# Performance work log

Hardware: AMD Instinct MI355X
Metric: run time of the kernel (lower is better)

## Reference

```python
import jax, jax.numpy as jnp
import numpy as np

B, T, C, H = 8, 2048, 1024, 64

def setup_inputs() -> dict:
    key = jax.random.key(0)
    kx, kk, kq, kv = jax.random.split(key, 4)
    x = jax.random.normal(kx, (B, T, C), dtype=jnp.float32)
    # nn.Linear(n_embed, head_size, bias=False) weights stored as [C, H] (already transposed)
    s = 1.0 / np.sqrt(C)
    Wk = jax.random.normal(kk, (C, H), dtype=jnp.float32) * s
    Wq = jax.random.normal(kq, (C, H), dtype=jnp.float32) * s
    Wv = jax.random.normal(kv, (C, H), dtype=jnp.float32) * s
    return {"x": x, "Wk": Wk, "Wq": Wq, "Wv": Wv}

def reference(x, Wk, Wq, Wv):
    Bq, Tq, Cq = x.shape
    k = jnp.einsum('btc,ch->bth', x, Wk)
    q = jnp.einsum('btc,ch->bth', x, Wq)
    v = jnp.einsum('btc,ch->bth', x, Wv)
    # NOTE: faithful to source, which MULTIPLIES by C**0.5 (not 1/sqrt(head_size))
    wei = jnp.einsum('bth,bsh->bts', q, k) * (Cq ** 0.5)  # [B,T,T]
    causal = jnp.tril(jnp.ones((Tq, Tq), dtype=bool))
    wei = jnp.where(causal, wei, -jnp.inf)
    wei = jax.nn.softmax(wei, axis=-1)
    out = jnp.einsum('bts,bsh->bth', wei, v)  # [B,T,H]
    return out
```

## Files before the change

### kernel.cpp

```cpp
#include <hip/hip_runtime.h>
#include <hip/hip_bf16.h>

#define TSEQ 2048
#define CDIM 1024
#define HDIM 64
#define NROW (8 * 2048)

typedef __attribute__((ext_vector_type(8))) short bf16x8;
typedef __attribute__((ext_vector_type(4))) float f32x4;
typedef __attribute__((ext_vector_type(4))) unsigned int u32x4;

__device__ __forceinline__ unsigned short f2bf(float f) {
    return __builtin_bit_cast(unsigned short, __float2bfloat16(f));
}
__device__ __forceinline__ float bf2f(unsigned short h) {
    unsigned int u = ((unsigned int)h) << 16;
    return __builtin_bit_cast(float, u);
}
__device__ __forceinline__ void split2(float v, unsigned short& h, unsigned short& l) {
    __hip_bfloat16 bh = __float2bfloat16(v);
    h = __builtin_bit_cast(unsigned short, bh);
    l = f2bf(v - __bfloat162float(bh));
}
__device__ __forceinline__ f32x4 mfma16(bf16x8 a, bf16x8 b, f32x4 c) {
    return __builtin_amdgcn_mfma_f32_16x16x32_bf16(a, b, c, 0, 0, 0);
}
__device__ __forceinline__ void gload_lds16(const unsigned short* g, unsigned short* l) {
    __builtin_amdgcn_global_load_lds(
        (const __attribute__((address_space(1))) unsigned int*)(g),
        (__attribute__((address_space(3))) unsigned int*)(l), 16, 0, 0);
}
__device__ __forceinline__ void gload_lds16f(const float* g, float* l) {
    __builtin_amdgcn_global_load_lds(
        (const __attribute__((address_space(1))) unsigned int*)(g),
        (__attribute__((address_space(3))) unsigned int*)(l), 16, 0, 0);
}

__global__ __launch_bounds__(256) void w_prep(
    const float* __restrict__ Wk, const float* __restrict__ Wq, const float* __restrict__ Wv,
    unsigned short* __restrict__ wThi, unsigned short* __restrict__ wTlo)
{
    __shared__ float tile[64][65];
    const int mm = blockIdx.x >> 4, kt = blockIdx.x & 15;
    const float* __restrict__ W = (mm == 0) ? Wk : (mm == 1) ? Wq : Wv;
    const int t = threadIdx.x;
    #pragma unroll
    for (int s = 0; s < 4; s++) {
        const int f = t + 256 * s;
        const int r = f >> 4, cq = f & 15;
        const float4 wv = *reinterpret_cast<const float4*>(&W[(long)(kt * 64 + r) * HDIM + 4 * cq]);
        tile[4 * cq + 0][r] = wv.x; tile[4 * cq + 1][r] = wv.y;
        tile[4 * cq + 2][r] = wv.z; tile[4 * cq + 3][r] = wv.w;
    }
    __syncthreads();
    const int n = t >> 2, seg = t & 3;
    unsigned short hi[16], lo[16];
    #pragma unroll
    for (int u = 0; u < 16; u++) split2(tile[n][16 * seg + u], hi[u], lo[u]);
    const long base = (long)(mm * 64 + n) * CDIM + kt * 64 + 16 * seg;
    *reinterpret_cast<uint4*>(&wThi[base + 0]) = *reinterpret_cast<uint4*>(&hi[0]);
    *reinterpret_cast<uint4*>(&wThi[base + 8]) = *reinterpret_cast<uint4*>(&hi[8]);
    *reinterpret_cast<uint4*>(&wTlo[base + 0]) = *reinterpret_cast<uint4*>(&lo[0]);
    *reinterpret_cast<uint4*>(&wTlo[base + 8]) = *reinterpret_cast<uint4*>(&lo[8]);
}

__global__ __launch_bounds__(256, 4) void proj_mfma(
    const float* __restrict__ x,
    const unsigned short* __restrict__ wThi, const unsigned short* __restrict__ wTlo,
    unsigned short* __restrict__ khi, unsigned short* __restrict__ klo,
    unsigned short* __restrict__ qhi, unsigned short* __restrict__ qlo,
    unsigned short* __restrict__ vt)
{
    extern __shared__ __align__(16) unsigned char smem[];
    const int t = threadIdx.x;
    const int lane = t & 63, w = t >> 6;
    const int r15 = lane & 15, g = lane >> 4;
    const int wr = w >> 1, wc = w & 1;
    const int bb8 = blockIdx.x & 7;
    const int u = blockIdx.x >> 3;
    const int jj = u >> 1, nh = u & 1;
    const long rowbase = (long)bb8 * TSEQ + jj * 64;

    long wsrc[3];
    #pragma unroll
    for (int q = 0; q < 3; q++) {
        const int s = t + 256 * q;
        const int row = s >> 3, gr = s & 7;
        wsrc[q] = (long)(nh * 96 + row) * CDIM + ((gr ^ (row & 7)) << 3);
    }
    long xsrc[4];
    #pragma unroll
    for (int q = 0; q < 4; q++) {
        const int s = t + 256 * q;
        const int row = s >> 4, gr = s & 15;
        xsrc[q] = (rowbase + row) * CDIM + ((gr ^ (row & 15)) << 2);
    }

    f32x4 acc[2][3];
    #pragma unroll
    for (int mt = 0; mt < 2; mt++)
        #pragma unroll
        for (int nt = 0; nt < 3; nt++) acc[mt][nt] = (f32x4){0.f, 0.f, 0.f, 0.f};

    auto stage = [&](int buf, int kc) {
        unsigned char* b = smem + buf * 40960;
        #pragma unroll
        for (int q = 0; q < 3; q++) {
            gload_lds16(wThi + wsrc[q] + kc, (unsigned short*)(b + (t + 256 * q) * 16));
            gload_lds16(wTlo + wsrc[q] + kc, (unsigned short*)(b + 12288 + (t + 256 * q) * 16));
        }
        #pragma unroll
        for (int q = 0; q < 4; q++)
            gload_lds16f(x + xsrc[q] + kc, (float*)(b + 24576 + (t + 256 * q) * 16));
    };

    auto compute = [&](int buf) {
        const unsigned short* wb = (const unsigned short*)(smem + buf * 40960);
        const float* xb = (const float*)(smem + buf * 40960 + 24576);
        bf16x8 ah[2][2], al[2][2];
        #pragma unroll
        for (int mt = 0; mt < 2; mt++) {
            const int rx = 32 * wr + 16 * mt + r15;
            #pragma unroll
            for (int ks = 0; ks < 2; ks++) {
                const f32x4 a0 = *reinterpret_cast<const f32x4*>(
                    xb + rx * 64 + (((8 * ks + 2 * g + 0) ^ r15) << 2));
                const f32x4 a1 = *reinterpret_cast<const f32x4*>(
                    xb + rx * 64 + (((8 * ks + 2 * g + 1) ^ r15) << 2));
                unsigned short h0,h1,h2,h3,h4,h5,h6,h7, l0,l1,l2,l3,l4,l5,l6,l7;
                split2(a0.x, h0, l0); split2(a0.y, h1, l1); split2(a0.z, h2, l2); split2(a0.w, h3, l3);
                split2(a1.x, h4, l4); split2(a1.y, h5, l5); split2(a1.z, h6, l6); split2(a1.w, h7, l7);
                ah[mt][ks] = (bf16x8){(short)h0,(short)h1,(short)h2,(short)h3,(short)h4,(short)h5,(short)h6,(short)h7};
                al[mt][ks] = (bf16x8){(short)l0,(short)l1,(short)l2,(short)l3,(short)l4,(short)l5,(short)l6,(short)l7};
            }
        }
        #pragma unroll
        for (int nt = 0; nt < 3; nt++) {
            const int rw = (3 * wc + nt) * 16 + r15;
            #pragma unroll
            for (int ks = 0; ks < 2; ks++) {
                const int go = (((4 * ks + g) ^ (rw & 7)) << 3);
                const bf16x8 bh = *reinterpret_cast<const bf16x8*>(wb + rw * 64 + go);
                const bf16x8 bl = *reinterpret_cast<const bf16x8*>(wb + 6144 + rw * 64 + go);
                #pragma unroll
                for (int mt = 0; mt < 2; mt++) {
                    acc[mt][nt] = mfma16(ah[mt][ks], bh, acc[mt][nt]);
                    acc[mt][nt] = mfma16(al[mt][ks], bh, acc[mt][nt]);
                    acc[mt][nt] = mfma16(ah[mt][ks], bl, acc[mt][nt]);
                }
            }
        }
    };

    stage(0, 0);
    __syncthreads();
    for (int j = 0; j < 16; ++j) {
        const int buf = j & 1;
        if (j < 15) stage(buf ^ 1, (j + 1) * 64);
        compute(buf);
        __syncthreads();
    }

    #pragma unroll
    for (int nt = 0; nt < 3; nt++) {
        const int ntg = 6 * nh + 3 * wc + nt;
        const int mat = ntg >> 2;
        const int colin = (ntg & 3) * 16 + r15;
        #pragma unroll
        for (int mt = 0; mt < 2; mt++) {
            const int rl = 32 * wr + 16 * mt + 4 * g;
            if (mat == 0) {
                #pragma unroll
                for (int reg = 0; reg < 4; reg++) {
                    unsigned short h, l;
                    split2(acc[mt][nt][reg], h, l);
                    const long idx = (rowbase + rl + reg) * HDIM + colin;
                    khi[idx] = h; klo[idx] = l;
                }
            } else if (mat == 1) {
                #pragma unroll
                for (int reg = 0; reg < 4; reg++) {
                    unsigned short h, l;
                    split2(acc[mt][nt][reg] * 32.0f, h, l);
                    const long idx = (rowbase + rl + reg) * HDIM + colin;
                    qhi[idx] = h; qlo[idx] = l;
                }
            } else {
                ushort4 pk;
                pk.x = f2bf(acc[mt][nt][0]); pk.y = f2bf(acc[mt][nt][1]);
                pk.z = f2bf(acc[mt][nt][2]); pk.w = f2bf(acc[mt][nt][3]);
                const long idx = ((long)bb8 * 64 + colin) * TSEQ + jj * 64 + rl;
                *reinterpret_cast<ushort4*>(&vt[idx]) = pk;
            }
        }
    }
}

__global__ __launch_bounds__(256, 3) void attn_part(
    const unsigned short* __restrict__ khi, const unsigned short* __restrict__ klo,
    const unsigned short* __restrict__ qhi, const unsigned short* __restrict__ qlo,
    const unsigned short* __restrict__ vt,
    float* __restrict__ po, float* __restrict__ pm, float* __restrict__ pl, int nsplit)
{
    __shared__ __align__(16) unsigned short ldsbuf[2][3 * 4096];
    const int t = threadIdx.x, w = t >> 6, lane = t & 63;
    const int r15 = lane & 15, g = lane >> 4;
    const int id = blockIdx.x;
    const int b = id & 7;
    const int u = id >> 3;
    const int t5 = u & 31, p = u >> 5;
    int j = (t5 & 1) ? 31 - (t5 >> 1) : (t5 >> 1);
    if (p & 1) j = 31 - j;
    const int n = j + 1;
    const int s = (p * n) / nsplit, e = ((p + 1) * n) / nsplit;
    const int pidx = (b * 32 + j) * nsplit + p;

    if (s >= e) {
        const int rr = t >> 2, cq = (t & 3) * 16;
        if ((t & 3) == 0) { pm[pidx * 64 + rr] = -3e38f; pl[pidx * 64 + rr] = 0.f; }
        const f32x4 z = (f32x4){0.f, 0.f, 0.f, 0.f};
        float* dst = &po[((long)pidx * 64 + rr) * 64 + cq];
        #pragma unroll
        for (int q = 0; q < 4; q++) *reinterpret_cast<f32x4*>(dst + 4 * q) = z;
        return;
    }

    const int row0 = t >> 3;
    const int ce = (((t & 7) ^ (row0 & 7)) << 3);
    const long bkey = (long)b * TSEQ;
    const long vrow = ((long)b * 64 + row0) * TSEQ;
    unsigned short* const lbT = &ldsbuf[0][0];

    auto stage = [&](int cur, int kb) {
        unsigned short* lb = lbT + cur * (3 * 4096) + t * 8;
        const long kgo  = (bkey + (long)kb * 64 + row0) * HDIM + ce;
        const long kgo2 = kgo + 32 * HDIM;
        const long vgo  = vrow + (long)kb * 64 + ce;
        const long vgo2 = vgo + 32L * TSEQ;
        gload_lds16(khi + kgo,  lb);
        gload_lds16(khi + kgo2, lb + 2048);
        gload_lds16(klo + kgo,  lb + 4096);
        gload_lds16(klo + kgo2, lb + 6144);
        gload_lds16(vt  + vgo,  lb + 8192);
        gload_lds16(vt  + vgo2, lb + 10240);
    };

    const long qrow = bkey + (long)j * 64 + 16 * w + r15;
    bf16x8 Qh[2], Ql[2];
    #pragma unroll
    for (int ks = 0; ks < 2; ks++) {
        Qh[ks] = *reinterpret_cast<const bf16x8*>(&qhi[qrow * HDIM + 32 * ks + 8 * g]);
        Ql[ks] = *reinterpret_cast<const bf16x8*>(&qlo[qrow * HDIM + 32 * ks + 8 * g]);
    }

    f32x4 o[4];
    #pragma unroll
    for (int ht = 0; ht < 4; ht++) o[ht] = (f32x4){0.f, 0.f, 0.f, 0.f};
    float m = -3e38f, lsum = 0.f;
    const int sw = (r15 & 7) << 4;
    const int c0 = ((16 * g) ^ sw) >> 1;
    const int c1 = ((16 * g + 64) ^ sw) >> 1;
    const int la = 16 * ((2 * g) & 3) + r15;
    const int lb_ = 16 * ((2 * g + 1) & 3) + r15;
    const int msel = g >> 1;

    stage(0, s);
    __syncthreads();

    for (int kb = s; kb < e; ++kb) {
        const int cur = (kb - s) & 1;
        if (kb + 1 < e) stage(cur ^ 1, kb + 1);
        const unsigned short* Kh = lbT + cur * (3 * 4096);
        const unsigned short* Kl = Kh + 4096;
        const unsigned short* Vb = Kh + 8192;
        const bool diag = (kb == j);

        f32x4 sc[4];
        #pragma unroll
        for (int mt = 0; mt < 4; mt++) {
            const bool valid = !diag || (mt <= w);
            f32x4 sv = valid ? (f32x4){0.f, 0.f, 0.f, 0.f}
                             : (f32x4){-1e30f, -1e30f, -1e30f, -1e30f};
            if (valid) {
                const int rb = (16 * mt + r15) * 64;
                const bf16x8 ah0 = *reinterpret_cast<const bf16x8*>(&Kh[rb + c0]);
                const bf16x8 ah1 = *reinterpret_cast<const bf16x8*>(&Kh[rb + c1]);
                const bf16x8 al0 = *reinterpret_cast<const bf16x8*>(&Kl[rb + c0]);
                const bf16x8 al1 = *reinterpret_cast<const bf16x8*>(&Kl[rb + c1]);
                sv = mfma16(ah0, Qh[0], sv);
                sv = mfma16(ah0, Ql[0], sv);
                sv = mfma16(al0, Qh[0], sv);
                sv = mfma16(ah1, Qh[1], sv);
                sv = mfma16(ah1, Ql[1], sv);
                sv = mfma16(al1, Qh[1], sv);
                if (diag && mt == w) {
                    #pragma unroll
                    for (int reg = 0; reg < 4; reg++)
                        if (4 * g + reg > r15) sv[reg] = -1e30f;
                }
            }
            sc[mt] = sv;
        }

        float bml = -3e38f;
        #pragma unroll
        for (int mt = 0; mt < 4; mt++)
            bml = fmaxf(bml, fmaxf(fmaxf(sc[mt][0], sc[mt][1]), fmaxf(sc[mt][2], sc[mt][3])));
        if (!__all(bml - m <= 8.0f)) {
            float bm = fmaxf(bml, __shfl_xor(bml, 16));
            bm = fmaxf(bm, __shfl_xor(bm, 32));
            const float mnew = fmaxf(m, bm);
            const float corr = __expf(m - mnew);
            lsum *= corr;
            #pragma unroll
            for (int ht = 0; ht < 4; ht++) o[ht] *= corr;
            m = mnew;
        }
        unsigned int pk[4][2];
        #pragma unroll
        for (int mt = 0; mt < 4; mt++) {
            const float p0 = __expf(sc[mt][0] - m);
            const float p1 = __expf(sc[mt][1] - m);
            const float p2 = __expf(sc[mt][2] - m);
            const float p3 = __expf(sc[mt][3] - m);
            lsum += (p0 + p1) + (p2 + p3);
            pk[mt][0] = (unsigned int)f2bf(p0) | ((unsigned int)f2bf(p1) << 16);
            pk[mt][1] = (unsigned int)f2bf(p2) | ((unsigned int)f2bf(p3) << 16);
        }
        #pragma unroll
        for (int ks = 0; ks < 2; ks++) {
            const int w0a = __shfl((int)pk[2 * ks + 0][0], la);
            const int w0b = __shfl((int)pk[2 * ks + 1][0], la);
            const int w1a = __shfl((int)pk[2 * ks + 0][1], la);
            const int w1b = __shfl((int)pk[2 * ks + 1][1], la);
            const int w2a = __shfl((int)pk[2 * ks + 0][0], lb_);
            const int w2b = __shfl((int)pk[2 * ks + 1][0], lb_);
            const int w3a = __shfl((int)pk[2 * ks + 0][1], lb_);
            const int w3b = __shfl((int)pk[2 * ks + 1][1], lb_);
            const u32x4 wv = {
                (unsigned int)(msel ? w0b : w0a), (unsigned int)(msel ? w1b : w1a),
                (unsigned int)(msel ? w2b : w2a), (unsigned int)(msel ? w3b : w3a)};
            const bf16x8 pb = __builtin_bit_cast(bf16x8, wv);
            const int cc = ks ? c1 : c0;
            #pragma unroll
            for (int ht = 0; ht < 4; ht++) {
                const bf16x8 av = *reinterpret_cast<const bf16x8*>(&Vb[(16 * ht + r15) * 64 + cc]);
                o[ht] = mfma16(av, pb, o[ht]);
            }
        }
        __syncthreads();
    }

    lsum += __shfl_xor(lsum, 16);
    lsum += __shfl_xor(lsum, 32);
    if (g == 0) { pm[pidx * 64 + 16 * w + r15] = m; pl[pidx * 64 + 16 * w + r15] = lsum; }
    #pragma unroll
    for (int ht = 0; ht < 4; ht++)
        *reinterpret_cast<f32x4*>(&po[((long)pidx * 64 + 16 * w + r15) * 64 + 16 * ht + 4 * g]) = o[ht];
}

__global__ __launch_bounds__(256) void attn_comb(
    const float* __restrict__ po, const float* __restrict__ pm, const float* __restrict__ pl,
    float* __restrict__ out, int nsplit)
{
    const int t = threadIdx.x;
    const int b = blockIdx.x & 7, j = blockIdx.x >> 3;
    const int r = t >> 2, cq = (t & 3) * 16;
    const int base = (b * 32 + j) * nsplit;

    float M = -3e38f;
    for (int p = 0; p < nsplit; ++p) M = fmaxf(M, pm[(base + p) * 64 + r]);
    float L = 0.f;
    f32x4 acc[4];
    #pragma unroll
    for (int q = 0; q < 4; q++) acc[q] = (f32x4){0.f, 0.f, 0.f, 0.f};
    for (int p = 0; p < nsplit; ++p) {
        const float wp = __expf(pm[(base + p) * 64 + r] - M);
        L += wp * pl[(base + p) * 64 + r];
        const float* src = &po[((long)(base + p) * 64 + r) * 64 + cq];
        #pragma unroll
        for (int q = 0; q < 4; q++) acc[q] += wp * *reinterpret_cast<const f32x4*>(src + 4 * q);
    }
    const float inv = 1.0f / L;
    float* dst = &out[((long)b * TSEQ + j * 64 + r) * HDIM + cq];
    #pragma unroll
    for (int q = 0; q < 4; q++) *reinterpret_cast<f32x4*>(dst + 4 * q) = acc[q] * inv;
}

extern "C" void kernel_launch(void* const* d_in, const int* in_sizes, int n_in,
                              void* d_out, int out_size, void* d_ws, size_t ws_size,
                              hipStream_t stream) {
    const float* x  = (const float*)d_in[0];
    const float* Wk = (const float*)d_in[1];
    const float* Wq = (const float*)d_in[2];
    const float* Wv = (const float*)d_in[3];
    float* outp = (float*)d_out;

    const size_t SZ = (size_t)NROW * HDIM;
    unsigned short* ws   = (unsigned short*)d_ws;
    unsigned short* khi  = ws;
    unsigned short* klo  = ws + 1 * SZ;
    unsigned short* qhi  = ws + 2 * SZ;
    unsigned short* qlo  = ws + 3 * SZ;
    unsigned short* vt   = ws + 4 * SZ;
    unsigned short* wThi = ws + 5 * SZ;
    unsigned short* wTlo = ws + 5 * SZ + 192 * 1024;

    const size_t base_bytes = (5 * SZ + 2 * 192 * 1024) * sizeof(unsigned short);
    int nsplit = 4;
    while (nsplit > 1 && base_bytes + (size_t)nsplit * 4325376 > ws_size) nsplit >>= 1;

    float* po = (float*)((char*)d_ws + base_bytes);
    float* pm = po + (size_t)256 * 64 * 64 * nsplit;
    float* pl = pm + (size_t)256 * 64 * nsplit;

    w_prep<<<48, 256, 0, stream>>>(Wk, Wq, Wv, wThi, wTlo);
    proj_mfma<<<512, 256, 81920, stream>>>(x, wThi, wTlo, khi, klo, qhi, qlo, vt);
    attn_part<<<dim3(256 * nsplit), 256, 0, stream>>>(khi, klo, qhi, qlo, vt, po, pm, pl, nsplit);
    attn_comb<<<256, 256, 0, stream>>>(po, pm, pl, outp, nsplit);
}
```

Before: 65.10 us.

## Triple-buffer projection GEMM with 32-wide K slices and vmcnt-based waits

The projection kernel now moves through K in 32-wide slices held in a 3-slot LDS ring, replacing the 64-wide double buffer. It waits on explicit vmcnt counts plus raw barriers, so two slices stay in flight while the current one is computed. The swizzles are reworked for the narrower rows, and shared memory per block drops from 80 KB to 60 KB, which may allow more resident blocks. The cost is twice as many loop iterations and barriers, and the hand-set vmcnt values must match the number of loads issued per stage exactly.

```diff
diff --git a/kernel.cpp b/kernel.cpp
--- a/kernel.cpp
+++ b/kernel.cpp
@@ -81,19 +81,22 @@
     const int jj = u >> 1, nh = u & 1;
     const long rowbase = (long)bb8 * TSEQ + jj * 64;
 
-    long wsrc[3];
+    const unsigned short* wsp[3];
     #pragma unroll
     for (int q = 0; q < 3; q++) {
         const int s = t + 256 * q;
+        const int lo = (s >= 384);
+        const int s3 = s - 384 * lo;
+        const int row = s3 >> 2, gr = s3 & 3;
+        wsp[q] = (lo ? wTlo : wThi) + (long)(nh * 96 + row) * CDIM
+               + ((gr ^ ((row >> 1) & 3)) << 3);
+    }
+    long xsrc[2];
+    #pragma unroll
+    for (int q = 0; q < 2; q++) {
+        const int s = t + 256 * q;
         const int row = s >> 3, gr = s & 7;
-        wsrc[q] = (long)(nh * 96 + row) * CDIM + ((gr ^ (row & 7)) << 3);
-    }
-    long xsrc[4];
-    #pragma unroll
-    for (int q = 0; q < 4; q++) {
-        const int s = t + 256 * q;
-        const int row = s >> 4, gr = s & 15;
-        xsrc[q] = (rowbase + row) * CDIM + ((gr ^ (row & 15)) << 2);
+        xsrc[q] = (rowbase + row) * CDIM + ((gr ^ (row & 7)) << 2);
     }
 
     f32x4 acc[2][3];
@@ -102,63 +105,63 @@
         #pragma unroll
         for (int nt = 0; nt < 3; nt++) acc[mt][nt] = (f32x4){0.f, 0.f, 0.f, 0.f};
 
-    auto stage = [&](int buf, int kc) {
-        unsigned char* b = smem + buf * 40960;
-        #pragma unroll
-        for (int q = 0; q < 3; q++) {
-            gload_lds16(wThi + wsrc[q] + kc, (unsigned short*)(b + (t + 256 * q) * 16));
-            gload_lds16(wTlo + wsrc[q] + kc, (unsigned short*)(b + 12288 + (t + 256 * q) * 16));
-        }
-        #pragma unroll
-        for (int q = 0; q < 4; q++)
-            gload_lds16f(x + xsrc[q] + kc, (float*)(b + 24576 + (t + 256 * q) * 16));
+    auto stage = [&](int sl, int kc) {
+        unsigned char* b = smem + sl * 20480;
+        #pragma unroll
+        for (int q = 0; q < 3; q++)
+            gload_lds16(wsp[q] + kc, (unsigned short*)(b + (t + 256 * q) * 16));
+        #pragma unroll
+        for (int q = 0; q < 2; q++)
+            gload_lds16f(x + xsrc[q] + kc, (float*)(b + 12288 + (t + 256 * q) * 16));
     };
 
-    auto compute = [&](int buf) {
-        const unsigned short* wb = (const unsigned short*)(smem + buf * 40960);
-        const float* xb = (const float*)(smem + buf * 40960 + 24576);
-        bf16x8 ah[2][2], al[2][2];
+    auto compute = [&](int sl) {
+        const unsigned short* wb = (const unsigned short*)(smem + sl * 20480);
+        const float* xb = (const float*)(smem + sl * 20480 + 12288);
+        bf16x8 ah[2], al[2];
         #pragma unroll
         for (int mt = 0; mt < 2; mt++) {
             const int rx = 32 * wr + 16 * mt + r15;
-            #pragma unroll
-            for (int ks = 0; ks < 2; ks++) {
-                const f32x4 a0 = *reinterpret_cast<const f32x4*>(
-                    xb + rx * 64 + (((8 * ks + 2 * g + 0) ^ r15) << 2));
-                const f32x4 a1 = *reinterpret_cast<const f32x4*>(
-                    xb + rx * 64 + (((8 * ks + 2 * g + 1) ^ r15) << 2));
-                unsigned short h0,h1,h2,h3,h4,h5,h6,h7, l0,l1,l2,l3,l4,l5,l6,l7;
-                split2(a0.x, h0, l0); split2(a0.y, h1, l1); split2(a0.z, h2, l2); split2(a0.w, h3, l3);
-                split2(a1.x, h4, l4); split2(a1.y, h5, l5); split2(a1.z, h6, l6); split2(a1.w, h7, l7);
-                ah[mt][ks] = (bf16x8){(short)h0,(short)h1,(short)h2,(short)h3,(short)h4,(short)h5,(short)h6,(short)h7};
-                al[mt][ks] = (bf16x8){(short)l0,(short)l1,(short)l2,(short)l3,(short)l4,(short)l5,(short)l6,(short)l7};
-            }
+            const int r7 = rx & 7;
+            const f32x4 a0 = *reinterpret_cast<const f32x4*>(
+                xb + rx * 32 + (((2 * g + 0) ^ r7) << 2));
+            const f32x4 a1 = *reinterpret_cast<const f32x4*>(
+                xb + rx * 32 + (((2 * g + 1) ^ r7) << 2));
+            unsigned short h0,h1,h2,h3,h4,h5,h6,h7, l0,l1,l2,l3,l4,l5,l6,l7;
+            split2(a0.x, h0, l0); split2(a0.y, h1, l1); split2(a0.z, h2, l2); split2(a0.w, h3, l3);
+            split2(a1.x, h4, l4); split2(a1.y, h5, l5); split2(a1.z, h6, l6); split2(a1.w, h7, l7);
+            ah[mt] = (bf16x8){(short)h0,(short)h1,(short)h2,(short)h3,(short)h4,(short)h5,(short)h6,(short)h7};
+            al[mt] = (bf16x8){(short)l0,(short)l1,(short)l2,(short)l3,(short)l4,(short)l5,(short)l6,(short)l7};
         }
         #pragma unroll
         for (int nt = 0; nt < 3; nt++) {
             const int rw = (3 * wc + nt) * 16 + r15;
+            const int go = ((g ^ ((rw >> 1) & 3)) << 3);
+            const bf16x8 bh = *reinterpret_cast<const bf16x8*>(wb + rw * 32 + go);
+            const bf16x8 bl = *reinterpret_cast<const bf16x8*>(wb + 3072 + rw * 32 + go);
             #pragma unroll
-            for (int ks = 0; ks < 2; ks++) {
-                const int go = (((4 * ks + g) ^ (rw & 7)) << 3);
-                const bf16x8 bh = *reinterpret_cast<const bf16x8*>(wb + rw * 64 + go);
-                const bf16x8 bl = *reinterpret_cast<const bf16x8*>(wb + 6144 + rw * 64 + go);
-                #pragma unroll
-                for (int mt = 0; mt < 2; mt++) {
-                    acc[mt][nt] = mfma16(ah[mt][ks], bh, acc[mt][nt]);
-                    acc[mt][nt] = mfma16(al[mt][ks], bh, acc[mt][nt]);
-                    acc[mt][nt] = mfma16(ah[mt][ks], bl, acc[mt][nt]);
-                }
+            for (int mt = 0; mt < 2; mt++) {
+                acc[mt][nt] = mfma16(ah[mt], bh, acc[mt][nt]);
+                acc[mt][nt] = mfma16(al[mt], bh, acc[mt][nt]);
+                acc[mt][nt] = mfma16(ah[mt], bl, acc[mt][nt]);
             }
         }
     };
 
     stage(0, 0);
-    __syncthreads();
-    for (int j = 0; j < 16; ++j) {
-        const int buf = j & 1;
-        if (j < 15) stage(buf ^ 1, (j + 1) * 64);
-        compute(buf);
-        __syncthreads();
+    stage(1, 32);
+
+    #pragma unroll 1
+    for (int j = 0; j < 32; ++j) {
+        if (j < 30) stage((j + 2) % 3, (j + 2) * 32);
+        if (j < 30)      { asm volatile("s_waitcnt vmcnt(10)" ::: "memory"); }
+        else if (j == 30){ asm volatile("s_waitcnt vmcnt(5)"  ::: "memory"); }
+        else             { asm volatile("s_waitcnt vmcnt(0)"  ::: "memory"); }
+        __builtin_amdgcn_s_barrier();
+        asm volatile("" ::: "memory");
+        compute(j % 3);
+        asm volatile("" ::: "memory");
+        __builtin_amdgcn_s_barrier();
     }
 
     #pragma unroll
@@ -415,7 +418,7 @@
     float* pl = pm + (size_t)256 * 64 * nsplit;
 
     w_prep<<<48, 256, 0, stream>>>(Wk, Wq, Wv, wThi, wTlo);
-    proj_mfma<<<512, 256, 81920, stream>>>(x, wThi, wTlo, khi, klo, qhi, qlo, vt);
+    proj_mfma<<<512, 256, 61440, stream>>>(x, wThi, wTlo, khi, klo, qhi, qlo, vt);
     attn_part<<<dim3(256 * nsplit), 256, 0, stream>>>(khi, klo, qhi, qlo, vt, po, pm, pl, nsplit);
     attn_comb<<<256, 256, 0, stream>>>(po, pm, pl, outp, nsplit);
 }
```

Result: no change. 65.70 us (+0.9%).
